# Kernel optimization log

Measured on AMD Instinct MI355X. Metric: run time of the kernel, lower is better.

Reference implementation:

```python
import jax, jax.numpy as jnp
import numpy as np

B, N, DIM = 4, 2048, 512
H, DH = 8, 64  # heads, dim_head; inner_dim = H*DH = 512
SCALE = DH ** -0.5
EPS = 1e-5


def _layer_norm(x, gamma):
    # LayerNorm with learned gamma and beta fixed to zeros (beta is a buffer)
    mu = jnp.mean(x, axis=-1, keepdims=True)
    var = jnp.var(x, axis=-1, keepdims=True)
    return (x - mu) * jax.lax.rsqrt(var + EPS) * gamma


def setup_inputs() -> dict:
    key = jax.random.key(0)
    ks = jax.random.split(key, 6)
    x = jax.random.normal(ks[0], (B, N, DIM), jnp.float32)
    mask = jax.random.bernoulli(ks[1], 0.9, (B, N))  # bool [b, n]
    gamma = jnp.ones((DIM,), jnp.float32)            # pre-attn LayerNorm gamma
    Wq = jax.random.normal(ks[2], (DIM, H * DH), jnp.float32) * 0.02
    Wkv = jax.random.normal(ks[3], (DIM, 2 * DH), jnp.float32) * 0.02  # shared single KV head (MQA)
    null_kv = jax.random.normal(ks[4], (2, DH), jnp.float32)
    Wout = jax.random.normal(ks[5], (H * DH, DIM), jnp.float32) * 0.02
    out_gamma = jnp.ones((DIM,), jnp.float32)        # post-proj LayerNorm gamma
    return {"x": x, "mask": mask, "gamma": gamma, "Wq": Wq, "Wkv": Wkv,
            "null_kv": null_kv, "Wout": Wout, "out_gamma": out_gamma}


def reference(x, mask, gamma, Wq, Wkv, null_kv, Wout, out_gamma):
    b, n, _ = x.shape
    xn = _layer_norm(x, gamma)
    # queries: per-head; keys/values: single shared head (multi-query)
    q = (xn @ Wq).reshape(b, n, H, DH).transpose(0, 2, 1, 3) * SCALE  # [b,h,n,d]
    kv = xn @ Wkv                                                     # [b,n,2d]
    k, v = kv[..., :DH], kv[..., DH:]                                 # [b,n,d]
    # prepend learned null key/value (attention sink) shared across batch
    nk = jnp.broadcast_to(null_kv[0], (b, 1, DH))
    nv = jnp.broadcast_to(null_kv[1], (b, 1, DH))
    k = jnp.concatenate([nk, k], axis=1)  # [b, n+1, d]
    v = jnp.concatenate([nv, v], axis=1)
    sim = jnp.einsum('bhid,bjd->bhij', q, k)  # [b,h,n,n+1]
    # mask padded with True for the null token, broadcast over heads/queries
    m = jnp.concatenate([jnp.ones((b, 1), bool), mask], axis=1)
    max_neg = -jnp.finfo(sim.dtype).max
    sim = jnp.where(m[:, None, None, :], sim, max_neg)
    attn = jax.nn.softmax(sim.astype(jnp.float32), axis=-1).astype(x.dtype)
    out = jnp.einsum('bhij,bjd->bhid', attn, v)       # [b,h,n,d]
    out = out.transpose(0, 2, 1, 3).reshape(b, n, H * DH)
    return _layer_norm(out @ Wout, out_gamma)
```

## Files before the change

kernel.cpp:

```cpp
#include <hip/hip_runtime.h>

typedef __attribute__((ext_vector_type(8)))  short bf16x8;
typedef __attribute__((ext_vector_type(4)))  float f32x4;
typedef __attribute__((ext_vector_type(16))) float f32x16;
typedef __attribute__((ext_vector_type(4)))  unsigned u32x4;

#define Nx 2048
#define CTXx 2049
#define KCAP 2112
#define QSCALE 0.18033688f

__device__ __forceinline__ short f2bs(float x){
    unsigned u = __builtin_bit_cast(unsigned, x);
    u = (u + 0x7fffu + ((u >> 16) & 1u)) >> 16;
    return (short)u;
}
__device__ __forceinline__ unsigned pack_trunc(float a, float b){
    return __builtin_amdgcn_perm(__builtin_bit_cast(unsigned, b),
                                 __builtin_bit_cast(unsigned, a), 0x07060302u);
}

__global__ void __launch_bounds__(256) ln1_kernel(const float* __restrict__ x,
                                                  const float* __restrict__ g,
                                                  short* __restrict__ out){
    int w = threadIdx.x >> 6, lane = threadIdx.x & 63;
    size_t row = (size_t)blockIdx.x * 4 + w;
    const float* xr = x + row * 512 + lane * 8;
    float4 a = *(const float4*)xr;
    float4 b = *(const float4*)(xr + 4);
    float s = a.x + a.y + a.z + a.w + b.x + b.y + b.z + b.w;
    float q = a.x*a.x + a.y*a.y + a.z*a.z + a.w*a.w
            + b.x*b.x + b.y*b.y + b.z*b.z + b.w*b.w;
    #pragma unroll
    for (int m = 1; m < 64; m <<= 1){ s += __shfl_xor(s, m, 64); q += __shfl_xor(q, m, 64); }
    float mu  = s * (1.f / 512.f);
    float var = fmaxf(q * (1.f / 512.f) - mu * mu, 0.f);
    float r   = rsqrtf(var + 1e-5f);
    const float* gr = g + lane * 8;
    float4 g0 = *(const float4*)gr;
    float4 g1 = *(const float4*)(gr + 4);
    bf16x8 o;
    o[0] = f2bs((a.x - mu) * r * g0.x); o[1] = f2bs((a.y - mu) * r * g0.y);
    o[2] = f2bs((a.z - mu) * r * g0.z); o[3] = f2bs((a.w - mu) * r * g0.w);
    o[4] = f2bs((b.x - mu) * r * g1.x); o[5] = f2bs((b.y - mu) * r * g1.y);
    o[6] = f2bs((b.z - mu) * r * g1.z); o[7] = f2bs((b.w - mu) * r * g1.w);
    *(bf16x8*)(out + row * 512 + lane * 8) = o;
}

__global__ void __launch_bounds__(256) ln2_kernel(const float* __restrict__ z,
                                                  const float* __restrict__ g,
                                                  float* __restrict__ out){
    int w = threadIdx.x >> 6, lane = threadIdx.x & 63;
    size_t row = (size_t)blockIdx.x * 4 + w;
    const float* xr = z + row * 512 + lane * 8;
    float4 a = *(const float4*)xr;
    float4 b = *(const float4*)(xr + 4);
    float s = a.x + a.y + a.z + a.w + b.x + b.y + b.z + b.w;
    float q = a.x*a.x + a.y*a.y + a.z*a.z + a.w*a.w
            + b.x*b.x + b.y*b.y + b.z*b.z + b.w*b.w;
    #pragma unroll
    for (int m = 1; m < 64; m <<= 1){ s += __shfl_xor(s, m, 64); q += __shfl_xor(q, m, 64); }
    float mu  = s * (1.f / 512.f);
    float var = fmaxf(q * (1.f / 512.f) - mu * mu, 0.f);
    float r   = rsqrtf(var + 1e-5f);
    const float* gr = g + lane * 8;
    float4 g0 = *(const float4*)gr;
    float4 g1 = *(const float4*)(gr + 4);
    float4 o0, o1;
    o0.x = (a.x - mu) * r * g0.x; o0.y = (a.y - mu) * r * g0.y;
    o0.z = (a.z - mu) * r * g0.z; o0.w = (a.w - mu) * r * g0.w;
    o1.x = (b.x - mu) * r * g1.x; o1.y = (b.y - mu) * r * g1.y;
    o1.z = (b.z - mu) * r * g1.z; o1.w = (b.w - mu) * r * g1.w;
    float* op = out + row * 512 + lane * 8;
    *(float4*)op = o0; *(float4*)(op + 4) = o1;
}

__global__ void __launch_bounds__(256) prep_kernel(const float* __restrict__ Wq,
                                                   const float* __restrict__ Wkv,
                                                   const float* __restrict__ Wout,
                                                   const float* __restrict__ nkv,
                                                   short* __restrict__ WcatT,
                                                   short* __restrict__ WoutT,
                                                   short* __restrict__ kb,
                                                   short* __restrict__ vbt){
    int bid = blockIdx.x, t = threadIdx.x;
    if (bid == 144){
        int b = t >> 6, d = t & 63;
        kb[((size_t)b * KCAP) * 64 + d] = f2bs(nkv[d]);
        vbt[((size_t)b * 64 + d) * KCAP + 0] = f2bs(nkv[64 + d]);
        return;
    }
    __shared__ float ls[64][65];
    bool isOut = (bid >= 80);
    int b2 = isOut ? bid - 80 : bid;
    int ntile = isOut ? (b2 & 7) : (b2 % 10);
    int ktile = isOut ? (b2 >> 3) : (b2 / 10);
    int n0 = ntile * 64, k0 = ktile * 64;
    #pragma unroll
    for (int rr = 0; rr < 64; rr += 16){
        int r = rr + (t >> 4), c = (t & 15) * 4;
        float4 v;
        if (isOut)            v = *(const float4*)(Wout + (size_t)(k0 + r) * 512 + n0 + c);
        else if (n0 < 512)    v = *(const float4*)(Wq   + (size_t)(k0 + r) * 512 + n0 + c);
        else                  v = *(const float4*)(Wkv  + (size_t)(k0 + r) * 128 + (n0 - 512) + c);
        ls[c + 0][r] = v.x; ls[c + 1][r] = v.y; ls[c + 2][r] = v.z; ls[c + 3][r] = v.w;
    }
    __syncthreads();
    int rn = t >> 2, kc = (t & 3) * 16;
    short tmp[16];
    #pragma unroll
    for (int j = 0; j < 16; j++) tmp[j] = f2bs(ls[rn][kc + j]);
    short* dst = (isOut ? WoutT : WcatT) + (size_t)(n0 + rn) * 512 + k0 + kc;
    *(int4*)dst       = *(int4*)&tmp[0];
    *(int4*)(dst + 8) = *(int4*)&tmp[8];
}

template<int MODE>
__global__ void __launch_bounds__(256, 2) gemm_mfma(const short* __restrict__ A,
                                                    const short* __restrict__ BwT,
                                                    short* __restrict__ qb,
                                                    short* __restrict__ kb,
                                                    short* __restrict__ vbt,
                                                    float* __restrict__ C){
    __shared__ short As[128][72];
    __shared__ short Bs[128][72];
    int t = threadIdx.x;
    int lane = t & 63, w = t >> 6;
    int l16 = lane & 15, quad = lane >> 4;
    int wm = w & 1, wn = w >> 1;
    int row0 = blockIdx.y * 128, col0 = blockIdx.x * 128;
    f32x4 acc[4][4];
    #pragma unroll
    for (int i = 0; i < 4; i++)
        #pragma unroll
        for (int j = 0; j < 4; j++) acc[i][j] = (f32x4){0.f, 0.f, 0.f, 0.f};
    int ar = t >> 1, ak = (t & 1) * 32;
    for (int k0 = 0; k0 < 512; k0 += 64){
        __syncthreads();
        {
            const short* ap = A + (size_t)(row0 + ar) * 512 + k0 + ak;
            int4 a0 = *(const int4*)(ap);
            int4 a1 = *(const int4*)(ap + 8);
            int4 a2 = *(const int4*)(ap + 16);
            int4 a3 = *(const int4*)(ap + 24);
            *(int4*)&As[ar][ak]      = a0;
            *(int4*)&As[ar][ak + 8]  = a1;
            *(int4*)&As[ar][ak + 16] = a2;
            *(int4*)&As[ar][ak + 24] = a3;
        }
        {
            const short* bp = BwT + (size_t)(col0 + ar) * 512 + k0 + ak;
            int4 b0 = *(const int4*)(bp);
            int4 b1 = *(const int4*)(bp + 8);
            int4 b2 = *(const int4*)(bp + 16);
            int4 b3 = *(const int4*)(bp + 24);
            *(int4*)&Bs[ar][ak]      = b0;
            *(int4*)&Bs[ar][ak + 8]  = b1;
            *(int4*)&Bs[ar][ak + 16] = b2;
            *(int4*)&Bs[ar][ak + 24] = b3;
        }
        __syncthreads();
        #pragma unroll
        for (int ks = 0; ks < 2; ks++){
            bf16x8 af[4], bfr[4];
            #pragma unroll
            for (int mt = 0; mt < 4; mt++)
                af[mt] = *(const bf16x8*)&As[wm * 64 + mt * 16 + l16][ks * 32 + quad * 8];
            #pragma unroll
            for (int nt = 0; nt < 4; nt++)
                bfr[nt] = *(const bf16x8*)&Bs[wn * 64 + nt * 16 + l16][ks * 32 + quad * 8];
            #pragma unroll
            for (int mt = 0; mt < 4; mt++)
                #pragma unroll
                for (int nt = 0; nt < 4; nt++)
                    acc[mt][nt] = __builtin_amdgcn_mfma_f32_16x16x32_bf16(af[mt], bfr[nt], acc[mt][nt], 0, 0, 0);
        }
    }
    #pragma unroll
    for (int mt = 0; mt < 4; mt++)
        #pragma unroll
        for (int nt = 0; nt < 4; nt++)
            #pragma unroll
            for (int r = 0; r < 4; r++){
                int row = row0 + wm * 64 + mt * 16 + quad * 4 + r;
                int col = col0 + wn * 64 + nt * 16 + l16;
                float v = acc[mt][nt][r];
                if (MODE == 0){
                    int bb = row >> 11, ii = row & 2047;
                    if (col < 512){
                        qb[(size_t)row * 512 + col] = f2bs(v * QSCALE);
                    } else if (col < 576){
                        kb[((size_t)bb * KCAP + ii + 1) * 64 + (col - 512)] = f2bs(v);
                    } else {
                        vbt[((size_t)bb * 64 + (col - 576)) * KCAP + ii + 1] = f2bs(v);
                    }
                } else {
                    C[(size_t)row * 512 + col] = v;
                }
            }
}

__global__ void __launch_bounds__(256, 2) attn_kernel(const short* __restrict__ qb,
                                                      const short* __restrict__ kb,
                                                      const short* __restrict__ vbt,
                                                      const int* __restrict__ mask,
                                                      short* __restrict__ ob){
    __shared__ short Ks[64][72];
    __shared__ short Vt[64][72];
    __shared__ float Ls[4][32];
    int t = threadIdx.x;
    int lane = t & 63, w = t >> 6;
    int n32 = lane & 31, hb = lane >> 5;
    int b = blockIdx.y, i0 = blockIdx.x * 16;
    int head = 2 * w + (n32 >> 4), row = i0 + (n32 & 15);
    bf16x8 qf[4];
    {
        const short* qp = qb + ((size_t)(b * Nx + row)) * 512 + head * 64 + hb * 8;
        #pragma unroll
        for (int ks = 0; ks < 4; ks++) qf[ks] = *(const bf16x8*)(qp + ks * 16);
    }
    f32x16 oacc[2];
    #pragma unroll
    for (int i = 0; i < 2; i++)
        #pragma unroll
        for (int j = 0; j < 16; j++) oacc[i][j] = 0.f;
    float lsum = 0.f;

    int skey = t >> 2, sd = (t & 3) * 16;
    int vd   = t >> 2, vk = (t & 3) * 16;
    const short* kgp = kb  + (size_t)b * KCAP * 64 + skey * 64 + sd;
    const short* vgp = vbt + ((size_t)b * 64 + vd) * KCAP + vk;
    const int* mrow = mask + b * Nx;

    int4 pk0, pk1, pv0, pv1;
    int mok;
    {
        pk0 = *(const int4*)(kgp);
        pk1 = *(const int4*)(kgp + 8);
        pv0 = *(const int4*)(vgp);
        pv1 = *(const int4*)(vgp + 8);
        int jg = lane;
        mok = (jg == 0) ? 1 : ((jg < CTXx) ? mrow[jg - 1] : 0);
    }
    for (int j0 = 0; j0 < KCAP; j0 += 64){
        __syncthreads();
        *(int4*)&Ks[skey][sd]     = pk0;
        *(int4*)&Ks[skey][sd + 8] = pk1;
        *(int4*)&Vt[vd][vk]       = make_int4(pv0.x, pv0.y, pv1.x, pv1.y);
        *(int4*)&Vt[vd][vk + 8]   = make_int4(pv0.z, pv0.w, pv1.z, pv1.w);
        unsigned long long bal = __ballot(mok != 0);
        __syncthreads();
        int jn = j0 + 64;
        if (jn < KCAP){
            pk0 = *(const int4*)(kgp + (size_t)jn * 64);
            pk1 = *(const int4*)(kgp + (size_t)jn * 64 + 8);
            pv0 = *(const int4*)(vgp + jn);
            pv1 = *(const int4*)(vgp + jn + 8);
            int jg = jn + lane;
            mok = (jg < CTXx) ? mrow[jg - 1] : 0;
        }
        f32x16 sf[2];
        #pragma unroll
        for (int i = 0; i < 2; i++)
            #pragma unroll
            for (int j = 0; j < 16; j++) sf[i][j] = 0.f;
        #pragma unroll
        for (int ks = 0; ks < 4; ks++){
            #pragma unroll
            for (int kt = 0; kt < 2; kt++){
                bf16x8 kf = *(const bf16x8*)&Ks[kt * 32 + n32][ks * 16 + hb * 8];
                sf[kt] = __builtin_amdgcn_mfma_f32_32x32x16_bf16(kf, qf[ks], sf[kt], 0, 0, 0);
            }
        }
        unsigned mlo = (unsigned)(bal >> (4 * hb));
        unsigned mhi = (unsigned)(bal >> (32 + 4 * hb));
        unsigned pg[8][2];
        #pragma unroll
        for (int kt = 0; kt < 2; kt++){
            unsigned mm = kt ? mhi : mlo;
            #pragma unroll
            for (int g4 = 0; g4 < 4; g4++){
                float p[4];
                #pragma unroll
                for (int tt = 0; tt < 4; tt++){
                    float e = __builtin_amdgcn_exp2f(sf[kt][g4 * 4 + tt]);
                    p[tt] = ((mm >> (8 * g4 + tt)) & 1u) ? e : 0.f;
                    lsum += p[tt];
                }
                pg[kt * 4 + g4][0] = pack_trunc(p[0], p[1]);
                pg[kt * 4 + g4][1] = pack_trunc(p[2], p[3]);
            }
        }
        #pragma unroll
        for (int s = 0; s < 4; s++){
            bf16x8 pa = __builtin_bit_cast(bf16x8,
                (u32x4){pg[2 * s][0], pg[2 * s][1], pg[2 * s + 1][0], pg[2 * s + 1][1]});
            #pragma unroll
            for (int nt = 0; nt < 2; nt++){
                bf16x8 vf = *(const bf16x8*)&Vt[nt * 32 + n32][s * 16 + hb * 8];
                oacc[nt] = __builtin_amdgcn_mfma_f32_32x32x16_bf16(pa, vf, oacc[nt], 0, 0, 0);
            }
        }
    }
    float L = lsum + __shfl_xor(lsum, 32, 64);
    if (hb == 0) Ls[w][n32] = 1.f / L;
    __syncthreads();
    #pragma unroll
    for (int nt = 0; nt < 2; nt++)
        #pragma unroll
        for (int r = 0; r < 16; r++){
            int hr = (r & 3) + 8 * (r >> 2) + 4 * hb;
            float o = oacc[nt][r] * Ls[w][hr];
            int grow = i0 + (hr & 15);
            int ghead = 2 * w + (hr >> 4);
            ob[((size_t)(b * Nx + grow)) * 512 + ghead * 64 + nt * 32 + n32] = f2bs(o);
        }
}

extern "C" void kernel_launch(void* const* d_in, const int* in_sizes, int n_in,
                              void* d_out, int out_size, void* d_ws, size_t ws_size,
                              hipStream_t stream){
    const float* x     = (const float*)d_in[0];
    const int*   mask  = (const int*)  d_in[1];
    const float* gamma = (const float*)d_in[2];
    const float* Wq    = (const float*)d_in[3];
    const float* Wkv   = (const float*)d_in[4];
    const float* nkv   = (const float*)d_in[5];
    const float* Wout  = (const float*)d_in[6];
    const float* og    = (const float*)d_in[7];
    float* out = (float*)d_out;

    short* xnb   = (short*)d_ws;
    short* qb    = xnb + (size_t)4194304;
    short* kb    = qb  + (size_t)4194304;
    short* vbt   = kb  + (size_t)540672;
    short* ob    = vbt + (size_t)540672;
    short* WcatT = ob  + (size_t)4194304;
    short* WoutT = WcatT + (size_t)327680;
    float* zb    = (float*)d_ws;

    ln1_kernel  <<<2048, 256, 0, stream>>>(x, gamma, xnb);
    prep_kernel <<<145, 256, 0, stream>>>(Wq, Wkv, Wout, nkv, WcatT, WoutT, kb, vbt);
    gemm_mfma<0><<<dim3(5, 64), 256, 0, stream>>>(xnb, WcatT, qb, kb, vbt, nullptr);
    attn_kernel <<<dim3(128, 4), 256, 0, stream>>>(qb, kb, vbt, mask, ob);
    gemm_mfma<1><<<dim3(4, 64), 256, 0, stream>>>(ob, WoutT, nullptr, nullptr, nullptr, zb);
    ln2_kernel  <<<2048, 256, 0, stream>>>(zb, og, out);
}
```

Before: 186.1 us.

## Double-buffer GEMM and attention LDS tiles, load K directly to registers, MFMA row sums

The GEMM kernel now uses two LDS buffers with register prefetch, so each k-step needs one barrier instead of two. The attention kernel drops the K tile from LDS and loads K fragments straight from global memory into registers. V is double-buffered in LDS with a single barrier per iteration. Softmax row sums now come from an extra MFMA against a ones vector, which removes the scalar accumulation, the shuffle and the LDS reduction. The trade-off is more registers and LDS per block, more global load traffic for K, and the sum is now taken over bf16-truncated probabilities.

```diff
diff --git a/kernel.cpp b/kernel.cpp
--- a/kernel.cpp
+++ b/kernel.cpp
@@ -122,8 +122,8 @@
                                                     short* __restrict__ kb,
                                                     short* __restrict__ vbt,
                                                     float* __restrict__ C){
-    __shared__ short As[128][72];
-    __shared__ short Bs[128][72];
+    __shared__ short As[2][128][72];
+    __shared__ short Bs[2][128][72];
     int t = threadIdx.x;
     int lane = t & 63, w = t >> 6;
     int l16 = lane & 15, quad = lane >> 4;
@@ -135,46 +135,46 @@
         #pragma unroll
         for (int j = 0; j < 4; j++) acc[i][j] = (f32x4){0.f, 0.f, 0.f, 0.f};
     int ar = t >> 1, ak = (t & 1) * 32;
+    const short* ap = A   + (size_t)(row0 + ar) * 512 + ak;
+    const short* bp = BwT + (size_t)(col0 + ar) * 512 + ak;
+    int4 a0 = *(const int4*)(ap);      int4 a1 = *(const int4*)(ap + 8);
+    int4 a2 = *(const int4*)(ap + 16); int4 a3 = *(const int4*)(ap + 24);
+    int4 b0 = *(const int4*)(bp);      int4 b1 = *(const int4*)(bp + 8);
+    int4 b2 = *(const int4*)(bp + 16); int4 b3 = *(const int4*)(bp + 24);
+    int p = 0;
     for (int k0 = 0; k0 < 512; k0 += 64){
+        *(int4*)&As[p][ar][ak]      = a0;
+        *(int4*)&As[p][ar][ak + 8]  = a1;
+        *(int4*)&As[p][ar][ak + 16] = a2;
+        *(int4*)&As[p][ar][ak + 24] = a3;
+        *(int4*)&Bs[p][ar][ak]      = b0;
+        *(int4*)&Bs[p][ar][ak + 8]  = b1;
+        *(int4*)&Bs[p][ar][ak + 16] = b2;
+        *(int4*)&Bs[p][ar][ak + 24] = b3;
         __syncthreads();
-        {
-            const short* ap = A + (size_t)(row0 + ar) * 512 + k0 + ak;
-            int4 a0 = *(const int4*)(ap);
-            int4 a1 = *(const int4*)(ap + 8);
-            int4 a2 = *(const int4*)(ap + 16);
-            int4 a3 = *(const int4*)(ap + 24);
-            *(int4*)&As[ar][ak]      = a0;
-            *(int4*)&As[ar][ak + 8]  = a1;
-            *(int4*)&As[ar][ak + 16] = a2;
-            *(int4*)&As[ar][ak + 24] = a3;
-        }
-        {
-            const short* bp = BwT + (size_t)(col0 + ar) * 512 + k0 + ak;
-            int4 b0 = *(const int4*)(bp);
-            int4 b1 = *(const int4*)(bp + 8);
-            int4 b2 = *(const int4*)(bp + 16);
-            int4 b3 = *(const int4*)(bp + 24);
-            *(int4*)&Bs[ar][ak]      = b0;
-            *(int4*)&Bs[ar][ak + 8]  = b1;
-            *(int4*)&Bs[ar][ak + 16] = b2;
-            *(int4*)&Bs[ar][ak + 24] = b3;
-        }
-        __syncthreads();
+        int kn = k0 + 64;
+        if (kn < 512){
+            a0 = *(const int4*)(ap + kn);      a1 = *(const int4*)(ap + kn + 8);
+            a2 = *(const int4*)(ap + kn + 16); a3 = *(const int4*)(ap + kn + 24);
+            b0 = *(const int4*)(bp + kn);      b1 = *(const int4*)(bp + kn + 8);
+            b2 = *(const int4*)(bp + kn + 16); b3 = *(const int4*)(bp + kn + 24);
+        }
         #pragma unroll
         for (int ks = 0; ks < 2; ks++){
             bf16x8 af[4], bfr[4];
             #pragma unroll
             for (int mt = 0; mt < 4; mt++)
-                af[mt] = *(const bf16x8*)&As[wm * 64 + mt * 16 + l16][ks * 32 + quad * 8];
+                af[mt] = *(const bf16x8*)&As[p][wm * 64 + mt * 16 + l16][ks * 32 + quad * 8];
             #pragma unroll
             for (int nt = 0; nt < 4; nt++)
-                bfr[nt] = *(const bf16x8*)&Bs[wn * 64 + nt * 16 + l16][ks * 32 + quad * 8];
+                bfr[nt] = *(const bf16x8*)&Bs[p][wn * 64 + nt * 16 + l16][ks * 32 + quad * 8];
             #pragma unroll
             for (int mt = 0; mt < 4; mt++)
                 #pragma unroll
                 for (int nt = 0; nt < 4; nt++)
                     acc[mt][nt] = __builtin_amdgcn_mfma_f32_16x16x32_bf16(af[mt], bfr[nt], acc[mt][nt], 0, 0, 0);
         }
+        p ^= 1;
     }
     #pragma unroll
     for (int mt = 0; mt < 4; mt++)
@@ -205,9 +205,7 @@
                                                       const short* __restrict__ vbt,
                                                       const int* __restrict__ mask,
                                                       short* __restrict__ ob){
-    __shared__ short Ks[64][72];
-    __shared__ short Vt[64][72];
-    __shared__ float Ls[4][32];
+    __shared__ short Vt[2][64][72];
     int t = threadIdx.x;
     int lane = t & 63, w = t >> 6;
     int n32 = lane & 31, hb = lane >> 5;
@@ -219,58 +217,56 @@
         #pragma unroll
         for (int ks = 0; ks < 4; ks++) qf[ks] = *(const bf16x8*)(qp + ks * 16);
     }
-    f32x16 oacc[2];
-    #pragma unroll
-    for (int i = 0; i < 2; i++)
-        #pragma unroll
-        for (int j = 0; j < 16; j++) oacc[i][j] = 0.f;
-    float lsum = 0.f;
-
-    int skey = t >> 2, sd = (t & 3) * 16;
-    int vd   = t >> 2, vk = (t & 3) * 16;
-    const short* kgp = kb  + (size_t)b * KCAP * 64 + skey * 64 + sd;
+    bf16x8 ones;
+    #pragma unroll
+    for (int j = 0; j < 8; j++) ones[j] = (short)0x3F80;
+    f32x16 oacc[2], lacc;
+    #pragma unroll
+    for (int j = 0; j < 16; j++){ oacc[0][j] = 0.f; oacc[1][j] = 0.f; lacc[j] = 0.f; }
+
+    int vd = t >> 2, vk = (t & 3) * 16;
     const short* vgp = vbt + ((size_t)b * 64 + vd) * KCAP + vk;
+    const short* kfb = kb  + (size_t)b * KCAP * 64 + (size_t)n32 * 64 + hb * 8;
     const int* mrow = mask + b * Nx;
 
-    int4 pk0, pk1, pv0, pv1;
-    int mok;
-    {
-        pk0 = *(const int4*)(kgp);
-        pk1 = *(const int4*)(kgp + 8);
-        pv0 = *(const int4*)(vgp);
-        pv1 = *(const int4*)(vgp + 8);
-        int jg = lane;
-        mok = (jg == 0) ? 1 : ((jg < CTXx) ? mrow[jg - 1] : 0);
-    }
+    int4 pv0 = *(const int4*)(vgp);
+    int4 pv1 = *(const int4*)(vgp + 8);
+    bf16x8 kfr[2][4];
+    #pragma unroll
+    for (int ks = 0; ks < 4; ks++){
+        kfr[0][ks] = *(const bf16x8*)(kfb + ks * 16);
+        kfr[1][ks] = *(const bf16x8*)(kfb + 2048 + ks * 16);
+    }
+    int mok = (lane == 0) ? 1 : ((lane < CTXx) ? mrow[lane - 1] : 0);
+
+    int p = 0;
     for (int j0 = 0; j0 < KCAP; j0 += 64){
+        *(int4*)&Vt[p][vd][vk]     = make_int4(pv0.x, pv0.y, pv1.x, pv1.y);
+        *(int4*)&Vt[p][vd][vk + 8] = make_int4(pv0.z, pv0.w, pv1.z, pv1.w);
         __syncthreads();
-        *(int4*)&Ks[skey][sd]     = pk0;
-        *(int4*)&Ks[skey][sd + 8] = pk1;
-        *(int4*)&Vt[vd][vk]       = make_int4(pv0.x, pv0.y, pv1.x, pv1.y);
-        *(int4*)&Vt[vd][vk + 8]   = make_int4(pv0.z, pv0.w, pv1.z, pv1.w);
         unsigned long long bal = __ballot(mok != 0);
-        __syncthreads();
+        f32x16 sf[2];
+        #pragma unroll
+        for (int i = 0; i < 2; i++)
+            #pragma unroll
+            for (int j = 0; j < 16; j++) sf[i][j] = 0.f;
+        #pragma unroll
+        for (int ks = 0; ks < 4; ks++){
+            sf[0] = __builtin_amdgcn_mfma_f32_32x32x16_bf16(kfr[0][ks], qf[ks], sf[0], 0, 0, 0);
+            sf[1] = __builtin_amdgcn_mfma_f32_32x32x16_bf16(kfr[1][ks], qf[ks], sf[1], 0, 0, 0);
+        }
         int jn = j0 + 64;
         if (jn < KCAP){
-            pk0 = *(const int4*)(kgp + (size_t)jn * 64);
-            pk1 = *(const int4*)(kgp + (size_t)jn * 64 + 8);
             pv0 = *(const int4*)(vgp + jn);
             pv1 = *(const int4*)(vgp + jn + 8);
+            const short* kp = kfb + (size_t)jn * 64;
+            #pragma unroll
+            for (int ks = 0; ks < 4; ks++){
+                kfr[0][ks] = *(const bf16x8*)(kp + ks * 16);
+                kfr[1][ks] = *(const bf16x8*)(kp + 2048 + ks * 16);
+            }
             int jg = jn + lane;
             mok = (jg < CTXx) ? mrow[jg - 1] : 0;
-        }
-        f32x16 sf[2];
-        #pragma unroll
-        for (int i = 0; i < 2; i++)
-            #pragma unroll
-            for (int j = 0; j < 16; j++) sf[i][j] = 0.f;
-        #pragma unroll
-        for (int ks = 0; ks < 4; ks++){
-            #pragma unroll
-            for (int kt = 0; kt < 2; kt++){
-                bf16x8 kf = *(const bf16x8*)&Ks[kt * 32 + n32][ks * 16 + hb * 8];
-                sf[kt] = __builtin_amdgcn_mfma_f32_32x32x16_bf16(kf, qf[ks], sf[kt], 0, 0, 0);
-            }
         }
         unsigned mlo = (unsigned)(bal >> (4 * hb));
         unsigned mhi = (unsigned)(bal >> (32 + 4 * hb));
@@ -280,41 +276,39 @@
             unsigned mm = kt ? mhi : mlo;
             #pragma unroll
             for (int g4 = 0; g4 < 4; g4++){
-                float p[4];
+                float pr[4];
                 #pragma unroll
                 for (int tt = 0; tt < 4; tt++){
                     float e = __builtin_amdgcn_exp2f(sf[kt][g4 * 4 + tt]);
-                    p[tt] = ((mm >> (8 * g4 + tt)) & 1u) ? e : 0.f;
-                    lsum += p[tt];
+                    pr[tt] = ((mm >> (8 * g4 + tt)) & 1u) ? e : 0.f;
                 }
-                pg[kt * 4 + g4][0] = pack_trunc(p[0], p[1]);
-                pg[kt * 4 + g4][1] = pack_trunc(p[2], p[3]);
+                pg[kt * 4 + g4][0] = pack_trunc(pr[0], pr[1]);
+                pg[kt * 4 + g4][1] = pack_trunc(pr[2], pr[3]);
             }
         }
         #pragma unroll
         for (int s = 0; s < 4; s++){
             bf16x8 pa = __builtin_bit_cast(bf16x8,
                 (u32x4){pg[2 * s][0], pg[2 * s][1], pg[2 * s + 1][0], pg[2 * s + 1][1]});
+            lacc = __builtin_amdgcn_mfma_f32_32x32x16_bf16(pa, ones, lacc, 0, 0, 0);
             #pragma unroll
             for (int nt = 0; nt < 2; nt++){
-                bf16x8 vf = *(const bf16x8*)&Vt[nt * 32 + n32][s * 16 + hb * 8];
+                bf16x8 vf = *(const bf16x8*)&Vt[p][nt * 32 + n32][s * 16 + hb * 8];
                 oacc[nt] = __builtin_amdgcn_mfma_f32_32x32x16_bf16(pa, vf, oacc[nt], 0, 0, 0);
             }
         }
-    }
-    float L = lsum + __shfl_xor(lsum, 32, 64);
-    if (hb == 0) Ls[w][n32] = 1.f / L;
-    __syncthreads();
-    #pragma unroll
-    for (int nt = 0; nt < 2; nt++)
-        #pragma unroll
-        for (int r = 0; r < 16; r++){
-            int hr = (r & 3) + 8 * (r >> 2) + 4 * hb;
-            float o = oacc[nt][r] * Ls[w][hr];
-            int grow = i0 + (hr & 15);
-            int ghead = 2 * w + (hr >> 4);
-            ob[((size_t)(b * Nx + grow)) * 512 + ghead * 64 + nt * 32 + n32] = f2bs(o);
-        }
+        p ^= 1;
+    }
+    #pragma unroll
+    for (int r = 0; r < 16; r++){
+        float linv = 1.f / lacc[r];
+        int hr = (r & 3) + 8 * (r >> 2) + 4 * hb;
+        int grow = i0 + (hr & 15);
+        int ghead = 2 * w + (hr >> 4);
+        short* op = ob + ((size_t)(b * Nx + grow)) * 512 + ghead * 64 + n32;
+        op[0]  = f2bs(oacc[0][r] * linv);
+        op[32] = f2bs(oacc[1][r] * linv);
+    }
 }
 
 extern "C" void kernel_launch(void* const* d_in, const int* in_sizes, int n_in,
```

Result: slower. 192.9 us (+3.7%).
